# Performance work log

Hardware: AMD Instinct MI355X
Metric: run time of the kernel (lower is better)

Reference implementation:

```python
import jax, jax.numpy as jnp
import numpy as np

B, N, E, F, FE = 4, 10000, 160000, 128, 16  # batch, nodes, edges, filters(=node feat dim), edge feat dim
EPS = 1e-3  # keras LayerNormalization default epsilon


def layernorm(x, gamma, beta):
    mu = jnp.mean(x, axis=-1, keepdims=True)
    var = jnp.mean(jnp.square(x - mu), axis=-1, keepdims=True)
    return (x - mu) * jax.lax.rsqrt(var + EPS) * gamma + beta


def setup_inputs() -> dict:
    key = jax.random.key(0)
    ks = jax.random.split(key, 8)
    nodes = jax.random.normal(ks[0], (B, N, F), dtype=jnp.float32)
    edge_features = jax.random.normal(ks[1], (B, E, FE), dtype=jnp.float32)
    edges = jax.random.randint(ks[2], (B, E, 2), 0, N, dtype=jnp.int32)
    edge_weights = jax.random.uniform(ks[3], (B, E, 1), dtype=jnp.float32)
    edge_dropout = jnp.ones((B, E, 2), dtype=jnp.float32)
    W_msg = jax.random.normal(ks[4], (2 * F + FE, F), dtype=jnp.float32) * 0.02
    b_msg = jnp.zeros((F,), jnp.float32)
    g_msg = jnp.ones((F,), jnp.float32)
    beta_msg = jnp.zeros((F,), jnp.float32)
    W_upd = jax.random.normal(ks[5], (2 * F, F), dtype=jnp.float32) * 0.02
    b_upd = jnp.zeros((F,), jnp.float32)
    g_upd = jnp.ones((F,), jnp.float32)
    beta_upd = jnp.zeros((F,), jnp.float32)
    return dict(nodes=nodes, edge_features=edge_features, edges=edges,
                edge_weights=edge_weights, edge_dropout=edge_dropout,
                W_msg=W_msg, b_msg=b_msg, g_msg=g_msg, beta_msg=beta_msg,
                W_upd=W_upd, b_upd=b_upd, g_upd=g_upd, beta_upd=beta_upd)


def reference(nodes, edge_features, edges, edge_weights, edge_dropout,
              W_msg, b_msg, g_msg, beta_msg, W_upd, b_upd, g_upd, beta_upd):
    n = nodes.shape[1]
    # gather both endpoints per edge: [B,E,2,F] -> [B,E,2F]
    gathered = jax.vmap(lambda nd, ed: nd[ed])(nodes, edges)
    msg_in = gathered.reshape(gathered.shape[0], gathered.shape[1], -1)
    msg_in = jnp.concatenate([msg_in, edge_features], axis=-1)
    # message MLP: Dense + GELU + LayerNorm
    h = jnp.einsum('bei,io->beo', msg_in, W_msg) + b_msg
    messages = layernorm(jax.nn.gelu(h, approximate=False), g_msg, beta_msg)
    weighted_messages = messages * edge_weights
    # scatter-sum to destination nodes (edge[:,1]), masked by dropout col 1
    dropped = weighted_messages * edge_dropout[..., 1:2]
    dst = edges[..., 1]
    aggregated = jax.vmap(lambda m, d: jax.ops.segment_sum(m, d, num_segments=n))(dropped, dst)
    # update: concat + Dense + GELU + LayerNorm
    combined = jnp.concatenate([nodes, aggregated], axis=-1)
    u = jnp.einsum('bni,io->bno', combined, W_upd) + b_upd
    updated_nodes = layernorm(jax.nn.gelu(u, approximate=False), g_upd, beta_upd)
    return updated_nodes
```

## Files before the change

kernel.cpp:

```cpp
#include <hip/hip_runtime.h>
#include <hip/hip_bf16.h>
#include <hip/hip_fp16.h>

#define BATCH   4
#define NNODES  10000
#define NEDGES  160000
#define FDIM    128
#define FEDIM   16
#define LNEPS   1e-3f
#define NTOTE   (BATCH * NEDGES)
#define NTOTN   (BATCH * NNODES)

typedef __attribute__((ext_vector_type(8))) short v8s;
typedef __attribute__((ext_vector_type(4))) float v4f;

#define AGG_BYTES   ((size_t)NTOTN * FDIM * 2)
#define CNT_OFF     AGG_BYTES
#define CNT_BYTES   ((size_t)NTOTN * 4)
#define CUR_OFF     (CNT_OFF + CNT_BYTES)
#define P_OFF       (CUR_OFF + CNT_BYTES)
#define P_BYTES     ((size_t)NTOTN * 256 * 2)
#define WTCAT_OFF   (P_OFF + P_BYTES)
#define WTUPD_OFF   (WTCAT_OFF + (size_t)256 * 128 * 2)
#define W3T_OFF     (WTUPD_OFF + (size_t)128 * 256 * 2)
#define REC_OFF     (W3T_OFF + (size_t)128 * 32 * 2)

static __device__ __forceinline__ unsigned short f2bf(float f) {
    __hip_bfloat16 h = __float2bfloat16(f);
    return *reinterpret_cast<unsigned short*>(&h);
}
static __device__ __forceinline__ float bfbits2f(unsigned bits16) {
    return __uint_as_float(bits16 << 16);
}

static __device__ __forceinline__ float gelu_f(float x) {
    float z = 0.7978845608028654f * (x + 0.044715f * x * x * x);
    float e = __expf(2.0f * z);
    float t = 1.0f - 2.0f / (e + 1.0f);
    return 0.5f * x * (1.0f + t);
}

static __device__ __forceinline__ bool is_bf16_mode(const void* gflag) {
    return ((*reinterpret_cast<const unsigned*>(gflag)) & 0xFFFFu) != 0u;
}
static __device__ __forceinline__ float ld_f(const void* p, long i, bool bf) {
    return bf ? (float)reinterpret_cast<const __hip_bfloat16*>(p)[i]
              : reinterpret_cast<const float*>(p)[i];
}
static __device__ __forceinline__ uint4 pack8(const float* p) {
    float4 f0 = *reinterpret_cast<const float4*>(p);
    float4 f1 = *reinterpret_cast<const float4*>(p + 4);
    uint4 o;
    o.x = f2bf(f0.x) | ((unsigned)f2bf(f0.y) << 16);
    o.y = f2bf(f0.z) | ((unsigned)f2bf(f0.w) << 16);
    o.z = f2bf(f1.x) | ((unsigned)f2bf(f1.y) << 16);
    o.w = f2bf(f1.z) | ((unsigned)f2bf(f1.w) << 16);
    return o;
}
static __device__ __forceinline__ uint4 h8_to_bf8(uint4 u) {
    unsigned w[4] = {u.x, u.y, u.z, u.w};
    uint4 o; unsigned r[4];
    #pragma unroll
    for (int q = 0; q < 4; q++) {
        __half lo = *reinterpret_cast<const __half*>(&w[q]);
        unsigned short hib = (unsigned short)(w[q] >> 16);
        __half hi = *reinterpret_cast<const __half*>(&hib);
        r[q] = f2bf(__half2float(lo)) | ((unsigned)f2bf(__half2float(hi)) << 16);
    }
    o.x = r[0]; o.y = r[1]; o.z = r[2]; o.w = r[3];
    return o;
}

#define NCAT (256 * 128)
#define NUPD (128 * 256)
#define NW3  (128 * 32)
__global__ void prep_weights(const void* __restrict__ Wmsg, const void* __restrict__ Wupd,
                             const void* __restrict__ gflag,
                             unsigned short* __restrict__ WtCat,
                             unsigned short* __restrict__ WtUpd,
                             unsigned short* __restrict__ W3t) {
    bool bf = is_bf16_mode(gflag);
    int i = blockIdx.x * 256 + threadIdx.x;
    if (i < NCAT) {
        int n = i >> 7, k = i & 127;
        int src = (n < 128) ? (k * 128 + n) : ((128 + k) * 128 + (n - 128));
        WtCat[i] = bf ? reinterpret_cast<const unsigned short*>(Wmsg)[src]
                      : f2bf(reinterpret_cast<const float*>(Wmsg)[src]);
    } else if (i < NCAT + NUPD) {
        int j = i - NCAT;
        int n = j >> 8, c = j & 255;
        WtUpd[j] = bf ? reinterpret_cast<const unsigned short*>(Wupd)[c * 128 + n]
                      : f2bf(reinterpret_cast<const float*>(Wupd)[c * 128 + n]);
    } else if (i < NCAT + NUPD + NW3) {
        int j = i - NCAT - NUPD;
        int n = j >> 5, k = j & 31;
        W3t[j] = (k < 16) ? (bf ? reinterpret_cast<const unsigned short*>(Wmsg)[(256 + k) * 128 + n]
                                : f2bf(reinterpret_cast<const float*>(Wmsg)[(256 + k) * 128 + n]))
                          : (unsigned short)0;
    }
}

__global__ __launch_bounds__(256) void edge_hist(const int* __restrict__ edges,
                                                 int* __restrict__ counts) {
    int gid = blockIdx.x * 256 + threadIdx.x;
    if (gid >= NTOTE) return;
    int b = gid / NEDGES;
    int2 e = reinterpret_cast<const int2*>(edges)[gid];
    atomicAdd(&counts[b * NNODES + e.y], 1);
}

__global__ __launch_bounds__(1024) void scan_kernel(const int* __restrict__ counts,
                                                    int* __restrict__ cursor) {
    __shared__ int part[1024];
    const int C = 40;
    int tid = threadIdx.x;
    int lo = tid * C;
    const bool act = (lo < NTOTN);
    int vals[C];
    int s = 0;
    if (act) {
        #pragma unroll
        for (int q = 0; q < C / 4; q++) {
            int4 t4 = *reinterpret_cast<const int4*>(counts + lo + q * 4);
            vals[q * 4 + 0] = t4.x; vals[q * 4 + 1] = t4.y;
            vals[q * 4 + 2] = t4.z; vals[q * 4 + 3] = t4.w;
            s += t4.x + t4.y + t4.z + t4.w;
        }
    }
    part[tid] = s;
    __syncthreads();
    for (int off = 1; off < 1024; off <<= 1) {
        int v = (tid >= off) ? part[tid - off] : 0;
        __syncthreads();
        part[tid] += v;
        __syncthreads();
    }
    int run = (tid > 0) ? part[tid - 1] : 0;
    if (act) {
        #pragma unroll
        for (int q = 0; q < C / 4; q++) {
            int4 o;
            o.x = run; run += vals[q * 4 + 0];
            o.y = run; run += vals[q * 4 + 1];
            o.z = run; run += vals[q * 4 + 2];
            o.w = run; run += vals[q * 4 + 3];
            *reinterpret_cast<int4*>(cursor + lo + q * 4) = o;
        }
    }
}

__global__ __launch_bounds__(256) void sort_scatter(
    const int*  __restrict__ edges,
    const void* __restrict__ ew,
    const void* __restrict__ ed,
    const void* __restrict__ gflag,
    int*        __restrict__ cursor,
    uint4*      __restrict__ rec)
{
    const bool bf = is_bf16_mode(gflag);
    int gid = blockIdx.x * 256 + threadIdx.x;
    if (gid >= NTOTE) return;
    int b = gid / NEDGES;
    long be = gid;
    int2 e = reinterpret_cast<const int2*>(edges)[gid];
    float w = ld_f(ew, be, bf) * ld_f(ed, be * 2 + 1, bf);
    int pos = atomicAdd(&cursor[b * NNODES + e.y], 1);
    rec[pos] = make_uint4((unsigned)(b * NNODES + e.x),
                          (unsigned)(b * NNODES + e.y),
                          __float_as_uint(w),
                          (unsigned)gid);
}

__global__ __launch_bounds__(256) void pg_kernel(
    const void* __restrict__ nodes,
    const void* __restrict__ bmsg,
    const void* __restrict__ gflag,
    const unsigned short* __restrict__ Wt,
    unsigned short*       __restrict__ P)
{
    const bool bf = is_bf16_mode(gflag);
    __shared__ unsigned short sW[128 * 40];
    __shared__ unsigned short sA[128 * 40];

    const int tid  = threadIdx.x;
    const int lane = tid & 63, wave = tid >> 6;
    const int c    = lane & 15, quad = lane >> 4;
    const int row0 = blockIdx.x * 128;
    const int half = blockIdx.y;
    const int NROWS = BATCH * NNODES;

    float bcol[8];
    #pragma unroll
    for (int nt = 0; nt < 8; nt++)
        bcol[nt] = (half == 0) ? ld_f(bmsg, nt * 16 + c, bf) : 0.f;

    v4f acc[2][8];
    #pragma unroll
    for (int mt = 0; mt < 2; mt++)
        #pragma unroll
        for (int nt = 0; nt < 8; nt++) { v4f z = {0.f, 0.f, 0.f, 0.f}; acc[mt][nt] = z; }

    for (int ks = 0; ks < 4; ks++) {
        #pragma unroll
        for (int q = tid; q < 512; q += 256) {
            int n = q >> 2, part = q & 3;
            *reinterpret_cast<uint4*>(&sW[n * 40 + part * 8]) =
                *reinterpret_cast<const uint4*>(Wt + (half * 128 + n) * 128 + ks * 32 + part * 8);
        }
        #pragma unroll
        for (int q = tid; q < 512; q += 256) {
            int t = q >> 2, part = q & 3;
            int row = row0 + t; if (row >= NROWS) row = NROWS - 1;
            long off = (size_t)row * FDIM + ks * 32 + part * 8;
            uint4 v = bf ? *reinterpret_cast<const uint4*>(reinterpret_cast<const unsigned short*>(nodes) + off)
                         : pack8(reinterpret_cast<const float*>(nodes) + off);
            *reinterpret_cast<uint4*>(&sA[t * 40 + part * 8]) = v;
        }
        __syncthreads();

        v8s a0 = *reinterpret_cast<const v8s*>(&sA[(wave * 32 + c) * 40 + quad * 8]);
        v8s a1 = *reinterpret_cast<const v8s*>(&sA[(wave * 32 + 16 + c) * 40 + quad * 8]);
        #pragma unroll
        for (int nt = 0; nt < 8; nt++) {
            v8s bfr = *reinterpret_cast<const v8s*>(&sW[(nt * 16 + c) * 40 + quad * 8]);
            acc[0][nt] = __builtin_amdgcn_mfma_f32_16x16x32_bf16(a0, bfr, acc[0][nt], 0, 0, 0);
            acc[1][nt] = __builtin_amdgcn_mfma_f32_16x16x32_bf16(a1, bfr, acc[1][nt], 0, 0, 0);
        }
        __syncthreads();
    }

    #pragma unroll
    for (int mt = 0; mt < 2; mt++)
        #pragma unroll
        for (int r = 0; r < 4; r++) {
            int row = row0 + wave * 32 + mt * 16 + quad * 4 + r;
            if (row < NROWS) {
                float v[8];
                #pragma unroll
                for (int nt = 0; nt < 8; nt++) v[nt] = acc[mt][nt][r] + bcol[nt];
                uint4 o;
                o.x = f2bf(v[0]) | ((unsigned)f2bf(v[1]) << 16);
                o.y = f2bf(v[2]) | ((unsigned)f2bf(v[3]) << 16);
                o.z = f2bf(v[4]) | ((unsigned)f2bf(v[5]) << 16);
                o.w = f2bf(v[6]) | ((unsigned)f2bf(v[7]) << 16);
                *reinterpret_cast<uint4*>(P + (size_t)row * 256 + half * 128 + c * 8) = o;
            }
        }
}

__global__ __launch_bounds__(256) void edge_kernel(
    const unsigned short* __restrict__ P,
    const uint4*          __restrict__ rec,
    const void* __restrict__ efeat,
    const unsigned short* __restrict__ W3t,
    const void* __restrict__ gmsg,
    const void* __restrict__ betamsg,
    __half*     __restrict__ agg)
{
    const bool bf = is_bf16_mode(gmsg);
    __shared__ int   sSrc[128], sDst[128], sEid[128];
    __shared__ float sWgt[128];

    const int tid  = threadIdx.x;
    const int e0   = blockIdx.x * 128;
    const int lane = tid & 63, wave = tid >> 6;
    const int c    = lane & 15, quad = lane >> 4;

    if (tid < 128) {
        uint4 hh = rec[e0 + tid];
        sSrc[tid] = (int)hh.x;
        sDst[tid] = (int)hh.y;
        sWgt[tid] = __uint_as_float(hh.z);
        sEid[tid] = (int)hh.w;
    }

    float gcol[8], becol[8];
    #pragma unroll
    for (int nt = 0; nt < 8; nt++) {
        gcol[nt]  = ld_f(gmsg, nt * 16 + c, bf);
        becol[nt] = ld_f(betamsg, nt * 16 + c, bf);
    }

    v8s bfrag[8];
    #pragma unroll
    for (int nt = 0; nt < 8; nt++)
        bfrag[nt] = *reinterpret_cast<const v8s*>(W3t + (nt * 16 + c) * 32 + quad * 8);

    v4f acc[2][8];
    #pragma unroll
    for (int mt = 0; mt < 2; mt++)
        #pragma unroll
        for (int nt = 0; nt < 8; nt++) { v4f z = {0.f, 0.f, 0.f, 0.f}; acc[mt][nt] = z; }

    __syncthreads();

    #pragma unroll
    for (int mt = 0; mt < 2; mt++) {
        v8s a = {0, 0, 0, 0, 0, 0, 0, 0};
        if (quad < 2) {
            int slot = wave * 32 + ((c >> 2) << 3) + mt * 4 + (c & 3);
            long eid = sEid[slot];
            uint4 u;
            if (bf) u = *reinterpret_cast<const uint4*>(
                        reinterpret_cast<const unsigned short*>(efeat) + eid * FEDIM + quad * 8);
            else    u = pack8(reinterpret_cast<const float*>(efeat) + eid * FEDIM + quad * 8);
            a = *reinterpret_cast<v8s*>(&u);
        }
        #pragma unroll
        for (int nt = 0; nt < 8; nt++)
            acc[mt][nt] = __builtin_amdgcn_mfma_f32_16x16x32_bf16(a, bfrag[nt], acc[mt][nt], 0, 0, 0);
    }

    const bool even = !(c & 1);
    float racc[8];
    int cur = -1;

    auto flushv = [&](int dstrow) {
        __half* aout = agg + (size_t)dstrow * FDIM;
        #pragma unroll
        for (int np = 0; np < 4; np++) {
            int nt = np * 2;
            float t0 = __shfl_xor(racc[nt], 1);
            float t1 = __shfl_xor(racc[nt + 1], 1);
            __half2 v = even ? __floats2half2_rn(racc[nt], t0)
                             : __floats2half2_rn(t1, racc[nt + 1]);
            int hoff = even ? (nt * 16 + c) : ((nt + 1) * 16 + c - 1);
            unsafeAtomicAdd(reinterpret_cast<__half2*>(aout + hoff), v);
        }
    };

    #pragma unroll
    for (int mt = 0; mt < 2; mt++) {
        uint4 U1[4], U2[4];
        #pragma unroll
        for (int r = 0; r < 4; r++) {
            int m = wave * 32 + quad * 8 + mt * 4 + r;
            U1[r] = *reinterpret_cast<const uint4*>(P + (size_t)sSrc[m] * 256 + c * 8);
            U2[r] = *reinterpret_cast<const uint4*>(P + (size_t)sDst[m] * 256 + 128 + c * 8);
        }
        #pragma unroll
        for (int r = 0; r < 4; r++) {
            int m = wave * 32 + quad * 8 + mt * 4 + r;
            unsigned w1[4] = {U1[r].x, U1[r].y, U1[r].z, U1[r].w};
            unsigned w2[4] = {U2[r].x, U2[r].y, U2[r].z, U2[r].w};
            float h[8];
            #pragma unroll
            for (int q = 0; q < 4; q++) {
                h[q * 2]     = bfbits2f(w1[q] & 0xFFFFu) + bfbits2f(w2[q] & 0xFFFFu) + acc[mt][q * 2][r];
                h[q * 2 + 1] = __uint_as_float(w1[q] & 0xFFFF0000u) + __uint_as_float(w2[q] & 0xFFFF0000u)
                               + acc[mt][q * 2 + 1][r];
            }
            float s = 0.f, sq = 0.f;
            #pragma unroll
            for (int nt = 0; nt < 8; nt++) {
                float g = gelu_f(h[nt]);
                h[nt] = g; s += g; sq += g * g;
            }
            #pragma unroll
            for (int off = 1; off < 16; off <<= 1) {
                s  += __shfl_xor(s, off);
                sq += __shfl_xor(sq, off);
            }
            float mu  = s * (1.0f / 128.0f);
            float var = sq * (1.0f / 128.0f) - mu * mu;
            float rs  = rsqrtf(var + LNEPS);
            float wgt = sWgt[m];
            int d = sDst[m];
            if (d != cur) {
                if (cur >= 0) flushv(cur);
                cur = d;
                #pragma unroll
                for (int nt = 0; nt < 8; nt++)
                    racc[nt] = ((h[nt] - mu) * rs * gcol[nt] + becol[nt]) * wgt;
            } else {
                #pragma unroll
                for (int nt = 0; nt < 8; nt++)
                    racc[nt] += ((h[nt] - mu) * rs * gcol[nt] + becol[nt]) * wgt;
            }
        }
    }
    flushv(cur);
}

__global__ __launch_bounds__(256) void upd_kernel(
    const void* __restrict__ nodes,
    const __half* __restrict__ agg,
    const unsigned short* __restrict__ Wt,
    const void* __restrict__ bupd,
    const void* __restrict__ gupd,
    const void* __restrict__ beupd,
    void*       __restrict__ out)
{
    const bool bf = is_bf16_mode(gupd);
    __shared__ unsigned short sW[128 * 40];
    __shared__ unsigned short sA[64 * 40];

    const int tid  = threadIdx.x;
    const int lane = tid & 63, wave = tid >> 6;
    const int c    = lane & 15, quad = lane >> 4;
    const int row0 = blockIdx.x * 64;

    float bcol[8], gcol[8], becol[8];
    #pragma unroll
    for (int nt = 0; nt < 8; nt++) {
        int col = nt * 16 + c;
        bcol[nt]  = ld_f(bupd, col, bf);
        gcol[nt]  = ld_f(gupd, col, bf);
        becol[nt] = ld_f(beupd, col, bf);
    }

    v4f acc[8];
    #pragma unroll
    for (int nt = 0; nt < 8; nt++) { v4f z = {0.f, 0.f, 0.f, 0.f}; acc[nt] = z; }

    for (int ks = 0; ks < 8; ks++) {
        #pragma unroll
        for (int q = tid; q < 512; q += 256) {
            int n = q >> 2, part = q & 3;
            *reinterpret_cast<uint4*>(&sW[n * 40 + part * 8]) =
                *reinterpret_cast<const uint4*>(Wt + n * 256 + ks * 32 + part * 8);
        }
        {
            int t = tid >> 2, part = tid & 3;
            int row = row0 + t;
            uint4 v;
            if (ks < 4) {
                long off = (size_t)row * FDIM + ks * 32 + part * 8;
                v = bf ? *reinterpret_cast<const uint4*>(reinterpret_cast<const unsigned short*>(nodes) + off)
                       : pack8(reinterpret_cast<const float*>(nodes) + off);
            } else {
                uint4 u = *reinterpret_cast<const uint4*>(
                    reinterpret_cast<const unsigned short*>(agg) + (size_t)row * FDIM + (ks - 4) * 32 + part * 8);
                v = h8_to_bf8(u);
            }
            *reinterpret_cast<uint4*>(&sA[t * 40 + part * 8]) = v;
        }
        __syncthreads();

        v8s a0 = *reinterpret_cast<const v8s*>(&sA[(wave * 16 + c) * 40 + quad * 8]);
        #pragma unroll
        for (int nt = 0; nt < 8; nt++) {
            v8s bfr = *reinterpret_cast<const v8s*>(&sW[(nt * 16 + c) * 40 + quad * 8]);
            acc[nt] = __builtin_amdgcn_mfma_f32_16x16x32_bf16(a0, bfr, acc[nt], 0, 0, 0);
        }
        __syncthreads();
    }

    float s[4] = {0, 0, 0, 0}, sq[4] = {0, 0, 0, 0};
    #pragma unroll
    for (int nt = 0; nt < 8; nt++) {
        v4f v = acc[nt];
        #pragma unroll
        for (int r = 0; r < 4; r++) {
            float g = gelu_f(v[r] + bcol[nt]);
            v[r] = g;
            s[r] += g; sq[r] += g * g;
        }
        acc[nt] = v;
    }
    #pragma unroll
    for (int off = 1; off < 16; off <<= 1) {
        #pragma unroll
        for (int r = 0; r < 4; r++) {
            s[r]  += __shfl_xor(s[r], off);
            sq[r] += __shfl_xor(sq[r], off);
        }
    }
    #pragma unroll
    for (int r = 0; r < 4; r++) {
        float mu  = s[r] * (1.0f / 128.0f);
        float var = sq[r] * (1.0f / 128.0f) - mu * mu;
        float rs  = rsqrtf(var + LNEPS);
        int row = row0 + wave * 16 + quad * 4 + r;
        #pragma unroll
        for (int nt = 0; nt < 8; nt++) {
            float y = (acc[nt][r] - mu) * rs * gcol[nt] + becol[nt];
            size_t oi = (size_t)row * FDIM + nt * 16 + c;
            if (bf) reinterpret_cast<__hip_bfloat16*>(out)[oi] = __float2bfloat16(y);
            else    reinterpret_cast<float*>(out)[oi] = y;
        }
    }
}

extern "C" void kernel_launch(void* const* d_in, const int* in_sizes, int n_in,
                              void* d_out, int out_size, void* d_ws, size_t ws_size,
                              hipStream_t stream)
{
    const void* nodes   = d_in[0];
    const void* efeat   = d_in[1];
    const int*  edges   = (const int*)d_in[2];
    const void* ew      = d_in[3];
    const void* ed      = d_in[4];
    const void* Wmsg    = d_in[5];
    const void* bmsg    = d_in[6];
    const void* gmsg    = d_in[7];
    const void* betamsg = d_in[8];
    const void* Wupd    = d_in[9];
    const void* bupd    = d_in[10];
    const void* gupd    = d_in[11];
    const void* betaupd = d_in[12];

    char* ws = (char*)d_ws;
    __half* agg          = (__half*)ws;
    int*    counts       = (int*)(ws + CNT_OFF);
    int*    cursor       = (int*)(ws + CUR_OFF);
    unsigned short* P    = (unsigned short*)(ws + P_OFF);
    unsigned short* WtCat= (unsigned short*)(ws + WTCAT_OFF);
    unsigned short* WtUpd= (unsigned short*)(ws + WTUPD_OFF);
    unsigned short* W3t  = (unsigned short*)(ws + W3T_OFF);
    uint4*          rec  = (uint4*)(ws + REC_OFF);

    hipMemsetAsync(agg, 0, AGG_BYTES + CNT_BYTES, stream);
    prep_weights<<<(NCAT + NUPD + NW3 + 255) / 256, 256, 0, stream>>>(
        Wmsg, Wupd, gmsg, WtCat, WtUpd, W3t);
    pg_kernel<<<dim3((NTOTN + 127) / 128, 2), 256, 0, stream>>>(
        nodes, bmsg, gmsg, WtCat, P);
    edge_hist<<<(NTOTE + 255) / 256, 256, 0, stream>>>(edges, counts);
    scan_kernel<<<1, 1024, 0, stream>>>(counts, cursor);
    sort_scatter<<<(NTOTE + 255) / 256, 256, 0, stream>>>(
        edges, ew, ed, gmsg, cursor, rec);
    edge_kernel<<<NTOTE / 128, 256, 0, stream>>>(
        P, rec, efeat, W3t, gmsg, betamsg, agg);
    upd_kernel<<<NTOTN / 64, 256, 0, stream>>>(
        nodes, agg, WtUpd, bupd, gupd, betaupd, d_out);
}
```

Before: 337.3 us.

## Switch edge aggregation to per-node CSR processing and use wave-shuffle scan

Replaces the edge-parallel message kernel, which flushed partial sums to the fp16 aggregate with atomics, with a node-parallel kernel. Each 16-lane group owns one destination node, walks its sorted incoming edges via counts and cursor, accumulates in registers and writes the aggregate once without atomics. That also drops the memset of the aggregate buffer, and the destination-side P row is loaded once per node instead of once per edge. The scan kernel swaps its LDS Hillis-Steele loop for wave shuffles. The risk is load imbalance from varying node degree, since each wave loops to the largest degree among its four nodes, plus less MFMA work per instruction.

Measured after the change: 387.1 us. 14.8% more time.

```diff
diff --git a/kernel.cpp b/kernel.cpp
--- a/kernel.cpp
+++ b/kernel.cpp
@@ -111,9 +111,9 @@
 
 __global__ __launch_bounds__(1024) void scan_kernel(const int* __restrict__ counts,
                                                     int* __restrict__ cursor) {
-    __shared__ int part[1024];
+    __shared__ int wsum[16];
     const int C = 40;
-    int tid = threadIdx.x;
+    int tid = threadIdx.x, lane = tid & 63, wave = tid >> 6;
     int lo = tid * C;
     const bool act = (lo < NTOTN);
     int vals[C];
@@ -127,15 +127,25 @@
             s += t4.x + t4.y + t4.z + t4.w;
         }
     }
-    part[tid] = s;
+    int sc = s;
+    #pragma unroll
+    for (int off = 1; off < 64; off <<= 1) {
+        int v = __shfl_up(sc, off);
+        if (lane >= off) sc += v;
+    }
+    if (lane == 63) wsum[wave] = sc;
     __syncthreads();
-    for (int off = 1; off < 1024; off <<= 1) {
-        int v = (tid >= off) ? part[tid - off] : 0;
-        __syncthreads();
-        part[tid] += v;
-        __syncthreads();
-    }
-    int run = (tid > 0) ? part[tid - 1] : 0;
+    if (wave == 0 && lane < 16) {
+        int t = wsum[lane];
+        #pragma unroll
+        for (int off = 1; off < 16; off <<= 1) {
+            int v = __shfl_up(t, off);
+            if (lane >= off) t += v;
+        }
+        wsum[lane] = t;
+    }
+    __syncthreads();
+    int run = (wave > 0 ? wsum[wave - 1] : 0) + (sc - s);
     if (act) {
         #pragma unroll
         for (int q = 0; q < C / 4; q++) {
@@ -248,31 +258,30 @@
         }
 }
 
-__global__ __launch_bounds__(256) void edge_kernel(
+__global__ __launch_bounds__(256) void node_kernel(
     const unsigned short* __restrict__ P,
     const uint4*          __restrict__ rec,
     const void* __restrict__ efeat,
+    const int*  __restrict__ counts,
+    const int*  __restrict__ rowend,
     const unsigned short* __restrict__ W3t,
     const void* __restrict__ gmsg,
     const void* __restrict__ betamsg,
     __half*     __restrict__ agg)
 {
     const bool bf = is_bf16_mode(gmsg);
-    __shared__ int   sSrc[128], sDst[128], sEid[128];
-    __shared__ float sWgt[128];
-
     const int tid  = threadIdx.x;
-    const int e0   = blockIdx.x * 128;
     const int lane = tid & 63, wave = tid >> 6;
     const int c    = lane & 15, quad = lane >> 4;
-
-    if (tid < 128) {
-        uint4 hh = rec[e0 + tid];
-        sSrc[tid] = (int)hh.x;
-        sDst[tid] = (int)hh.y;
-        sWgt[tid] = __uint_as_float(hh.z);
-        sEid[tid] = (int)hh.w;
-    }
+    const int node = blockIdx.x * 16 + wave * 4 + quad;
+
+    const int deg = counts[node];
+    const int s0  = rowend[node] - deg;
+
+    const int aq   = c >> 2;
+    const int s0a  = __shfl(s0, aq * 16);
+    const int dega = __shfl(deg, aq * 16);
+    const int aslot = c & 3;
 
     float gcol[8], becol[8];
     #pragma unroll
@@ -286,69 +295,57 @@
     for (int nt = 0; nt < 8; nt++)
         bfrag[nt] = *reinterpret_cast<const v8s*>(W3t + (nt * 16 + c) * 32 + quad * 8);
 
-    v4f acc[2][8];
-    #pragma unroll
-    for (int mt = 0; mt < 2; mt++)
-        #pragma unroll
-        for (int nt = 0; nt < 8; nt++) { v4f z = {0.f, 0.f, 0.f, 0.f}; acc[mt][nt] = z; }
-
-    __syncthreads();
-
-    #pragma unroll
-    for (int mt = 0; mt < 2; mt++) {
+    float p2[8];
+    {
+        uint4 U2 = *reinterpret_cast<const uint4*>(P + (size_t)node * 256 + 128 + c * 8);
+        unsigned w2[4] = {U2.x, U2.y, U2.z, U2.w};
+        #pragma unroll
+        for (int q = 0; q < 4; q++) {
+            p2[q * 2]     = bfbits2f(w2[q] & 0xFFFFu);
+            p2[q * 2 + 1] = __uint_as_float(w2[q] & 0xFFFF0000u);
+        }
+    }
+
+    float racc[8];
+    #pragma unroll
+    for (int nt = 0; nt < 8; nt++) racc[nt] = 0.f;
+
+    int m = deg;
+    m = max(m, __shfl_xor(m, 16));
+    m = max(m, __shfl_xor(m, 32));
+    const int iters = (m + 3) >> 2;
+
+    for (int it = 0; it < iters; ++it) {
         v8s a = {0, 0, 0, 0, 0, 0, 0, 0};
-        if (quad < 2) {
-            int slot = wave * 32 + ((c >> 2) << 3) + mt * 4 + (c & 3);
-            long eid = sEid[slot];
+        const int apos = it * 4 + aslot;
+        if (quad < 2 && apos < dega) {
+            long eid = (long)rec[s0a + apos].w;
             uint4 u;
             if (bf) u = *reinterpret_cast<const uint4*>(
                         reinterpret_cast<const unsigned short*>(efeat) + eid * FEDIM + quad * 8);
             else    u = pack8(reinterpret_cast<const float*>(efeat) + eid * FEDIM + quad * 8);
             a = *reinterpret_cast<v8s*>(&u);
         }
+        v4f acc[8];
+        #pragma unroll
+        for (int nt = 0; nt < 8; nt++) { v4f z = {0.f, 0.f, 0.f, 0.f}; acc[nt] = z; }
         #pragma unroll
         for (int nt = 0; nt < 8; nt++)
-            acc[mt][nt] = __builtin_amdgcn_mfma_f32_16x16x32_bf16(a, bfrag[nt], acc[mt][nt], 0, 0, 0);
-    }
-
-    const bool even = !(c & 1);
-    float racc[8];
-    int cur = -1;
-
-    auto flushv = [&](int dstrow) {
-        __half* aout = agg + (size_t)dstrow * FDIM;
-        #pragma unroll
-        for (int np = 0; np < 4; np++) {
-            int nt = np * 2;
-            float t0 = __shfl_xor(racc[nt], 1);
-            float t1 = __shfl_xor(racc[nt + 1], 1);
-            __half2 v = even ? __floats2half2_rn(racc[nt], t0)
-                             : __floats2half2_rn(t1, racc[nt + 1]);
-            int hoff = even ? (nt * 16 + c) : ((nt + 1) * 16 + c - 1);
-            unsafeAtomicAdd(reinterpret_cast<__half2*>(aout + hoff), v);
-        }
-    };
-
-    #pragma unroll
-    for (int mt = 0; mt < 2; mt++) {
-        uint4 U1[4], U2[4];
+            acc[nt] = __builtin_amdgcn_mfma_f32_16x16x32_bf16(a, bfrag[nt], acc[nt], 0, 0, 0);
+
         #pragma unroll
         for (int r = 0; r < 4; r++) {
-            int m = wave * 32 + quad * 8 + mt * 4 + r;
-            U1[r] = *reinterpret_cast<const uint4*>(P + (size_t)sSrc[m] * 256 + c * 8);
-            U2[r] = *reinterpret_cast<const uint4*>(P + (size_t)sDst[m] * 256 + 128 + c * 8);
-        }
-        #pragma unroll
-        for (int r = 0; r < 4; r++) {
-            int m = wave * 32 + quad * 8 + mt * 4 + r;
-            unsigned w1[4] = {U1[r].x, U1[r].y, U1[r].z, U1[r].w};
-            unsigned w2[4] = {U2[r].x, U2[r].y, U2[r].z, U2[r].w};
+            const int pos = it * 4 + r;
+            if (pos >= deg) continue;
+            uint4 rr = rec[s0 + pos];
+            float wgt = __uint_as_float(rr.z);
+            uint4 U1 = *reinterpret_cast<const uint4*>(P + (size_t)rr.x * 256 + c * 8);
+            unsigned w1[4] = {U1.x, U1.y, U1.z, U1.w};
             float h[8];
             #pragma unroll
             for (int q = 0; q < 4; q++) {
-                h[q * 2]     = bfbits2f(w1[q] & 0xFFFFu) + bfbits2f(w2[q] & 0xFFFFu) + acc[mt][q * 2][r];
-                h[q * 2 + 1] = __uint_as_float(w1[q] & 0xFFFF0000u) + __uint_as_float(w2[q] & 0xFFFF0000u)
-                               + acc[mt][q * 2 + 1][r];
+                h[q * 2]     = bfbits2f(w1[q] & 0xFFFFu) + p2[q * 2] + acc[q * 2][r];
+                h[q * 2 + 1] = __uint_as_float(w1[q] & 0xFFFF0000u) + p2[q * 2 + 1] + acc[q * 2 + 1][r];
             }
             float s = 0.f, sq = 0.f;
             #pragma unroll
@@ -364,22 +361,24 @@
             float mu  = s * (1.0f / 128.0f);
             float var = sq * (1.0f / 128.0f) - mu * mu;
             float rs  = rsqrtf(var + LNEPS);
-            float wgt = sWgt[m];
-            int d = sDst[m];
-            if (d != cur) {
-                if (cur >= 0) flushv(cur);
-                cur = d;
-                #pragma unroll
-                for (int nt = 0; nt < 8; nt++)
-                    racc[nt] = ((h[nt] - mu) * rs * gcol[nt] + becol[nt]) * wgt;
-            } else {
-                #pragma unroll
-                for (int nt = 0; nt < 8; nt++)
-                    racc[nt] += ((h[nt] - mu) * rs * gcol[nt] + becol[nt]) * wgt;
-            }
-        }
-    }
-    flushv(cur);
+            #pragma unroll
+            for (int nt = 0; nt < 8; nt++)
+                racc[nt] += ((h[nt] - mu) * rs * gcol[nt] + becol[nt]) * wgt;
+        }
+    }
+
+    const bool even = !(c & 1);
+    __half* aout = agg + (size_t)node * FDIM;
+    #pragma unroll
+    for (int np = 0; np < 4; np++) {
+        int nt = np * 2;
+        float t0 = __shfl_xor(racc[nt], 1);
+        float t1 = __shfl_xor(racc[nt + 1], 1);
+        __half2 v = even ? __floats2half2_rn(racc[nt], t0)
+                         : __floats2half2_rn(t1, racc[nt + 1]);
+        int hoff = even ? (nt * 16 + c) : ((nt + 1) * 16 + c - 1);
+        *reinterpret_cast<__half2*>(aout + hoff) = v;
+    }
 }
 
 __global__ __launch_bounds__(256) void upd_kernel(
@@ -510,7 +509,7 @@
     unsigned short* W3t  = (unsigned short*)(ws + W3T_OFF);
     uint4*          rec  = (uint4*)(ws + REC_OFF);
 
-    hipMemsetAsync(agg, 0, AGG_BYTES + CNT_BYTES, stream);
+    hipMemsetAsync(counts, 0, CNT_BYTES, stream);
     prep_weights<<<(NCAT + NUPD + NW3 + 255) / 256, 256, 0, stream>>>(
         Wmsg, Wupd, gmsg, WtCat, WtUpd, W3t);
     pg_kernel<<<dim3((NTOTN + 127) / 128, 2), 256, 0, stream>>>(
@@ -519,8 +518,8 @@
     scan_kernel<<<1, 1024, 0, stream>>>(counts, cursor);
     sort_scatter<<<(NTOTE + 255) / 256, 256, 0, stream>>>(
         edges, ew, ed, gmsg, cursor, rec);
-    edge_kernel<<<NTOTE / 128, 256, 0, stream>>>(
-        P, rec, efeat, W3t, gmsg, betamsg, agg);
+    node_kernel<<<NTOTN / 16, 256, 0, stream>>>(
+        P, rec, efeat, counts, cursor, W3t, gmsg, betamsg, agg);
     upd_kernel<<<NTOTN / 64, 256, 0, stream>>>(
         nodes, agg, WtUpd, bupd, gupd, betaupd, d_out);
 }
```

## Fuse memset and histogram into other kernels, pack edge features into sorted records

Applied to the files above, without the earlier changes.

Zeroing of the aggregation and count buffers moves into the weight-prep kernel, replacing the separate memset. The edge histogram moves into pg_kernel, which removes two launches. The scan now uses wave shuffles instead of a 1024-step LDS scan with many barriers. The sort pass copies each edge's features into a 48-byte record, so edge_kernel reads them contiguously in sorted order, with no indirect efeat gather and no LDS staging. The cost is triple the record storage and write traffic, and the workspace must be large enough to hold it.

Result: faster. 324.1 us (-3.9%).

```diff
diff --git a/kernel.cpp b/kernel.cpp
--- a/kernel.cpp
+++ b/kernel.cpp
@@ -74,13 +74,18 @@
 #define NCAT (256 * 128)
 #define NUPD (128 * 256)
 #define NW3  (128 * 32)
-__global__ void prep_weights(const void* __restrict__ Wmsg, const void* __restrict__ Wupd,
-                             const void* __restrict__ gflag,
-                             unsigned short* __restrict__ WtCat,
-                             unsigned short* __restrict__ WtUpd,
-                             unsigned short* __restrict__ W3t) {
+__global__ __launch_bounds__(256) void init_kernel(
+    const void* __restrict__ Wmsg, const void* __restrict__ Wupd,
+    const void* __restrict__ gflag,
+    unsigned short* __restrict__ WtCat,
+    unsigned short* __restrict__ WtUpd,
+    unsigned short* __restrict__ W3t,
+    uint4* __restrict__ aggz,
+    uint4* __restrict__ cntz) {
     bool bf = is_bf16_mode(gflag);
     int i = blockIdx.x * 256 + threadIdx.x;
+    aggz[i] = make_uint4(0, 0, 0, 0);
+    if (i < (int)(CNT_BYTES / 16)) cntz[i] = make_uint4(0, 0, 0, 0);
     if (i < NCAT) {
         int n = i >> 7, k = i & 127;
         int src = (n < 128) ? (k * 128 + n) : ((128 + k) * 128 + (n - 128));
@@ -100,20 +105,11 @@
     }
 }
 
-__global__ __launch_bounds__(256) void edge_hist(const int* __restrict__ edges,
-                                                 int* __restrict__ counts) {
-    int gid = blockIdx.x * 256 + threadIdx.x;
-    if (gid >= NTOTE) return;
-    int b = gid / NEDGES;
-    int2 e = reinterpret_cast<const int2*>(edges)[gid];
-    atomicAdd(&counts[b * NNODES + e.y], 1);
-}
-
 __global__ __launch_bounds__(1024) void scan_kernel(const int* __restrict__ counts,
                                                     int* __restrict__ cursor) {
-    __shared__ int part[1024];
+    __shared__ int wsum[16];
     const int C = 40;
-    int tid = threadIdx.x;
+    int tid = threadIdx.x, lane = tid & 63, wave = tid >> 6;
     int lo = tid * C;
     const bool act = (lo < NTOTN);
     int vals[C];
@@ -127,15 +123,25 @@
             s += t4.x + t4.y + t4.z + t4.w;
         }
     }
-    part[tid] = s;
+    int sc = s;
+    #pragma unroll
+    for (int off = 1; off < 64; off <<= 1) {
+        int v = __shfl_up(sc, off);
+        if (lane >= off) sc += v;
+    }
+    if (lane == 63) wsum[wave] = sc;
     __syncthreads();
-    for (int off = 1; off < 1024; off <<= 1) {
-        int v = (tid >= off) ? part[tid - off] : 0;
-        __syncthreads();
-        part[tid] += v;
-        __syncthreads();
-    }
-    int run = (tid > 0) ? part[tid - 1] : 0;
+    if (wave == 0 && lane < 16) {
+        int t = wsum[lane];
+        #pragma unroll
+        for (int off = 1; off < 16; off <<= 1) {
+            int v = __shfl_up(t, off);
+            if (lane >= off) t += v;
+        }
+        wsum[lane] = t;
+    }
+    __syncthreads();
+    int run = (wave > 0 ? wsum[wave - 1] : 0) + (sc - s);
     if (act) {
         #pragma unroll
         for (int q = 0; q < C / 4; q++) {
@@ -153,6 +159,7 @@
     const int*  __restrict__ edges,
     const void* __restrict__ ew,
     const void* __restrict__ ed,
+    const void* __restrict__ efeat,
     const void* __restrict__ gflag,
     int*        __restrict__ cursor,
     uint4*      __restrict__ rec)
@@ -164,11 +171,22 @@
     long be = gid;
     int2 e = reinterpret_cast<const int2*>(edges)[gid];
     float w = ld_f(ew, be, bf) * ld_f(ed, be * 2 + 1, bf);
+    uint4 h0, h1;
+    if (bf) {
+        const unsigned short* ep = reinterpret_cast<const unsigned short*>(efeat) + be * FEDIM;
+        h0 = *reinterpret_cast<const uint4*>(ep);
+        h1 = *reinterpret_cast<const uint4*>(ep + 8);
+    } else {
+        const float* ep = reinterpret_cast<const float*>(efeat) + be * FEDIM;
+        h0 = pack8(ep);
+        h1 = pack8(ep + 8);
+    }
     int pos = atomicAdd(&cursor[b * NNODES + e.y], 1);
-    rec[pos] = make_uint4((unsigned)(b * NNODES + e.x),
-                          (unsigned)(b * NNODES + e.y),
-                          __float_as_uint(w),
-                          (unsigned)gid);
+    rec[(size_t)pos * 3 + 0] = h0;
+    rec[(size_t)pos * 3 + 1] = h1;
+    rec[(size_t)pos * 3 + 2] = make_uint4((unsigned)(b * NNODES + e.x),
+                                          (unsigned)(b * NNODES + e.y),
+                                          __float_as_uint(w), 0u);
 }
 
 __global__ __launch_bounds__(256) void pg_kernel(
@@ -176,6 +194,8 @@
     const void* __restrict__ bmsg,
     const void* __restrict__ gflag,
     const unsigned short* __restrict__ Wt,
+    const int*  __restrict__ edges,
+    int*        __restrict__ counts,
     unsigned short*       __restrict__ P)
 {
     const bool bf = is_bf16_mode(gflag);
@@ -188,6 +208,17 @@
     const int row0 = blockIdx.x * 128;
     const int half = blockIdx.y;
     const int NROWS = BATCH * NNODES;
+
+    if (half == 0) {
+        #pragma unroll
+        for (int k = 0; k < 8; k++) {
+            int g = blockIdx.x * 2048 + k * 256 + tid;
+            if (g < NTOTE) {
+                int2 e = reinterpret_cast<const int2*>(edges)[g];
+                atomicAdd(&counts[(g / NEDGES) * NNODES + e.y], 1);
+            }
+        }
+    }
 
     float bcol[8];
     #pragma unroll
@@ -251,28 +282,16 @@
 __global__ __launch_bounds__(256) void edge_kernel(
     const unsigned short* __restrict__ P,
     const uint4*          __restrict__ rec,
-    const void* __restrict__ efeat,
     const unsigned short* __restrict__ W3t,
     const void* __restrict__ gmsg,
     const void* __restrict__ betamsg,
     __half*     __restrict__ agg)
 {
     const bool bf = is_bf16_mode(gmsg);
-    __shared__ int   sSrc[128], sDst[128], sEid[128];
-    __shared__ float sWgt[128];
-
     const int tid  = threadIdx.x;
-    const int e0   = blockIdx.x * 128;
     const int lane = tid & 63, wave = tid >> 6;
     const int c    = lane & 15, quad = lane >> 4;
-
-    if (tid < 128) {
-        uint4 hh = rec[e0 + tid];
-        sSrc[tid] = (int)hh.x;
-        sDst[tid] = (int)hh.y;
-        sWgt[tid] = __uint_as_float(hh.z);
-        sEid[tid] = (int)hh.w;
-    }
+    const int we0  = blockIdx.x * 128 + wave * 32;
 
     float gcol[8], becol[8];
     #pragma unroll
@@ -292,18 +311,12 @@
         #pragma unroll
         for (int nt = 0; nt < 8; nt++) { v4f z = {0.f, 0.f, 0.f, 0.f}; acc[mt][nt] = z; }
 
-    __syncthreads();
-
     #pragma unroll
     for (int mt = 0; mt < 2; mt++) {
         v8s a = {0, 0, 0, 0, 0, 0, 0, 0};
         if (quad < 2) {
-            int slot = wave * 32 + ((c >> 2) << 3) + mt * 4 + (c & 3);
-            long eid = sEid[slot];
-            uint4 u;
-            if (bf) u = *reinterpret_cast<const uint4*>(
-                        reinterpret_cast<const unsigned short*>(efeat) + eid * FEDIM + quad * 8);
-            else    u = pack8(reinterpret_cast<const float*>(efeat) + eid * FEDIM + quad * 8);
+            int slot = we0 + ((c >> 2) << 3) + mt * 4 + (c & 3);
+            uint4 u = rec[(size_t)slot * 3 + quad];
             a = *reinterpret_cast<v8s*>(&u);
         }
         #pragma unroll
@@ -331,16 +344,18 @@
 
     #pragma unroll
     for (int mt = 0; mt < 2; mt++) {
+        uint4 H[4];
+        #pragma unroll
+        for (int r = 0; r < 4; r++)
+            H[r] = rec[(size_t)(we0 + quad * 8 + mt * 4 + r) * 3 + 2];
         uint4 U1[4], U2[4];
         #pragma unroll
         for (int r = 0; r < 4; r++) {
-            int m = wave * 32 + quad * 8 + mt * 4 + r;
-            U1[r] = *reinterpret_cast<const uint4*>(P + (size_t)sSrc[m] * 256 + c * 8);
-            U2[r] = *reinterpret_cast<const uint4*>(P + (size_t)sDst[m] * 256 + 128 + c * 8);
+            U1[r] = *reinterpret_cast<const uint4*>(P + (size_t)H[r].x * 256 + c * 8);
+            U2[r] = *reinterpret_cast<const uint4*>(P + (size_t)H[r].y * 256 + 128 + c * 8);
         }
         #pragma unroll
         for (int r = 0; r < 4; r++) {
-            int m = wave * 32 + quad * 8 + mt * 4 + r;
             unsigned w1[4] = {U1[r].x, U1[r].y, U1[r].z, U1[r].w};
             unsigned w2[4] = {U2[r].x, U2[r].y, U2[r].z, U2[r].w};
             float h[8];
@@ -364,8 +379,8 @@
             float mu  = s * (1.0f / 128.0f);
             float var = sq * (1.0f / 128.0f) - mu * mu;
             float rs  = rsqrtf(var + LNEPS);
-            float wgt = sWgt[m];
-            int d = sDst[m];
+            float wgt = __uint_as_float(H[r].z);
+            int d = (int)H[r].y;
             if (d != cur) {
                 if (cur >= 0) flushv(cur);
                 cur = d;
@@ -510,17 +525,15 @@
     unsigned short* W3t  = (unsigned short*)(ws + W3T_OFF);
     uint4*          rec  = (uint4*)(ws + REC_OFF);
 
-    hipMemsetAsync(agg, 0, AGG_BYTES + CNT_BYTES, stream);
-    prep_weights<<<(NCAT + NUPD + NW3 + 255) / 256, 256, 0, stream>>>(
-        Wmsg, Wupd, gmsg, WtCat, WtUpd, W3t);
-    pg_kernel<<<dim3((NTOTN + 127) / 128, 2), 256, 0, stream>>>(
-        nodes, bmsg, gmsg, WtCat, P);
-    edge_hist<<<(NTOTE + 255) / 256, 256, 0, stream>>>(edges, counts);
+    init_kernel<<<2500, 256, 0, stream>>>(
+        Wmsg, Wupd, gmsg, WtCat, WtUpd, W3t, (uint4*)agg, (uint4*)counts);
+    pg_kernel<<<dim3(313, 2), 256, 0, stream>>>(
+        nodes, bmsg, gmsg, WtCat, edges, counts, P);
     scan_kernel<<<1, 1024, 0, stream>>>(counts, cursor);
     sort_scatter<<<(NTOTE + 255) / 256, 256, 0, stream>>>(
-        edges, ew, ed, gmsg, cursor, rec);
+        edges, ew, ed, efeat, gmsg, cursor, rec);
     edge_kernel<<<NTOTE / 128, 256, 0, stream>>>(
-        P, rec, efeat, W3t, gmsg, betamsg, agg);
+        P, rec, W3t, gmsg, betamsg, agg);
     upd_kernel<<<NTOTN / 64, 256, 0, stream>>>(
         nodes, agg, WtUpd, bupd, gupd, betaupd, d_out);
 }
```
